# Performance work log

Measured on AMD Instinct MI355X. Metric: run time of the kernel, lower is better.

Reference implementation:

```python
import jax, jax.numpy as jnp
import numpy as np

D_MODEL, NHEAD, D_K = 512, 8, 64
MIN_RBF, MAX_RBF = 0.1, 0.9
MIN_SPREAD, MAX_SPREAD, BASE = 1.0, 6.0, 20.0
LN_EPS = 1e-5


def _layernorm(x, w, b):
    mu = jnp.mean(x, axis=-1, keepdims=True)
    var = jnp.var(x, axis=-1, keepdims=True)
    return (x - mu) * jax.lax.rsqrt(var + LN_EPS) * w + b


def setup_inputs() -> dict:
    key = jax.random.key(0)
    ks = jax.random.split(key, 10)
    B, N = 1, 2048
    inp = {
        "q": jax.random.normal(ks[0], (B, N, D_MODEL), jnp.float32),
        "k": jax.random.normal(ks[1], (B, N, D_MODEL), jnp.float32),
        "v": jax.random.normal(ks[2], (B, N, D_MODEL), jnp.float32),
        "coords": jax.random.normal(ks[3], (B, N, 3), jnp.float32) * 3.0,
        "key_padding_mask": jnp.zeros((B, N), bool),
        # learned params (torch.randn init for projections, LN defaults)
        "q_proj": jax.random.normal(ks[4], (NHEAD, D_MODEL, D_K), jnp.float32),
        "k_proj": jax.random.normal(ks[5], (NHEAD, D_MODEL, D_K), jnp.float32),
        "v_proj": jax.random.normal(ks[6], (NHEAD, D_MODEL, D_K), jnp.float32),
        "q_ln_w": jnp.ones((D_K,), jnp.float32), "q_ln_b": jnp.zeros((D_K,), jnp.float32),
        "k_ln_w": jnp.ones((D_K,), jnp.float32), "k_ln_b": jnp.zeros((D_K,), jnp.float32),
        "v_ln_w": jnp.ones((D_K,), jnp.float32), "v_ln_b": jnp.zeros((D_K,), jnp.float32),
        "out_w": jax.random.normal(ks[7], (D_MODEL, D_MODEL), jnp.float32) / np.sqrt(D_MODEL),
        "out_b": jnp.zeros((D_MODEL,), jnp.float32),
    }
    return inp


def reference(q, k, v, coords, key_padding_mask,
              q_proj, k_proj, v_proj,
              q_ln_w, q_ln_b, k_ln_w, k_ln_b, v_ln_w, v_ln_b,
              out_w, out_b):
    B, N, _ = q.shape
    # per-head projections: [B,H,N,dk]
    Q = _layernorm(jnp.einsum('bnd,hdk->bhnk', q, q_proj), q_ln_w, q_ln_b)
    K = _layernorm(jnp.einsum('bnd,hdk->bhnk', k, k_proj), k_ln_w, k_ln_b)
    V = _layernorm(jnp.einsum('bnd,hdk->bhnk', v, v_proj), v_ln_w, v_ln_b)

    # head-specific gaussian spreads (torch.logspace(0,1,H,base) semantics)
    spreads = MIN_SPREAD + (MAX_SPREAD - MIN_SPREAD) * (BASE ** jnp.linspace(0.0, 1.0, NHEAD) - 1.0) / (BASE - 1.0)

    # pairwise squared distances [B,N,N] -> per-head RBF [B,H,N,N]
    d2 = jnp.sum((coords[:, :, None, :] - coords[:, None, :, :]) ** 2, axis=-1)
    rbf = jnp.exp(-d2[:, None, :, :] / (2.0 * spreads[None, :, None, None] ** 2))
    rbf = jnp.clip(rbf, MIN_RBF, MAX_RBF)

    # RBF-modulated scaled dot-product attention
    scores = jnp.einsum('bhik,bhjk->bhij', Q, K) / np.sqrt(D_K) * rbf
    scores = jnp.where(key_padding_mask[:, None, None, :], -1e9, scores)
    P = jax.nn.softmax(scores, axis=-1)
    out = jnp.einsum('bhij,bhjk->bhik', P, V)  # [B,H,N,dk]

    # torch: out.permute(0,2,3,1).reshape(B,N,d_model)
    out = jnp.transpose(out, (0, 2, 3, 1)).reshape(B, N, D_MODEL)
    return out @ out_w.T + out_b
```

## Files before the change

### kernel.cpp

```cpp
#include <hip/hip_runtime.h>
#include <math.h>

#define N_TOK 2048
#define D_MODEL 512
#define NHEAD 8
#define DK 64
#define LOG2E 1.44269504f
#define QSCALE 0.18033688f

typedef __attribute__((ext_vector_type(8))) short short8;
typedef __attribute__((ext_vector_type(4))) short short4v;
typedef __attribute__((ext_vector_type(4))) float f32x4;

__device__ __forceinline__ short f2bf(float x) {
    unsigned u = __float_as_uint(x);
    u = (u + 0x7fffu + ((u >> 16) & 1u)) >> 16;
    return (short)u;
}

__device__ __forceinline__ unsigned cvt_pk_bf16(float lo, float hi) {
    unsigned r;
    asm("v_cvt_pk_bf16_f32 %0, %1, %2" : "=v"(r) : "v"(lo), "v"(hi));
    return r;
}

__device__ __forceinline__ float head_c(int h) {
    float tt = (float)h * (1.0f / 7.0f);
    float sp = 1.0f + 5.0f * (__builtin_exp2f(tt * 4.3219281f) - 1.0f) * (1.0f / 19.0f);
    return -LOG2E / (2.0f * sp * sp);
}

__global__ __launch_bounds__(256) void convert_x_kernel(
    const float* __restrict__ q, const float* __restrict__ k,
    const float* __restrict__ v, short* __restrict__ Xbf)
{
    int i = blockIdx.x * 256 + threadIdx.x;
    int t = i >> 17;
    int rem = i & 131071;
    const float4* src = (const float4*)(t == 0 ? q : (t == 1 ? k : v));
    float4 a = src[rem * 2], b = src[rem * 2 + 1];
    short8 o;
    o[0] = f2bf(a.x); o[1] = f2bf(a.y); o[2] = f2bf(a.z); o[3] = f2bf(a.w);
    o[4] = f2bf(b.x); o[5] = f2bf(b.y); o[6] = f2bf(b.z); o[7] = f2bf(b.w);
    *(short8*)(Xbf + (size_t)i * 8) = o;
}

__global__ __launch_bounds__(256) void prep_w_kernel(
    const float* __restrict__ qp, const float* __restrict__ kp,
    const float* __restrict__ vp, const float* __restrict__ ow,
    short* __restrict__ Wt, short* __restrict__ Wo)
{
    const int z = blockIdx.z, t = threadIdx.x;
    if (z == 3) {
        int m0 = blockIdx.x * 64, j0 = blockIdx.y * 64;
        for (int i = t; i < 4096; i += 256) {
            int r = i >> 6, c = i & 63;
            size_t idx = (size_t)(m0 + r) * 512 + j0 + c;
            Wo[idx] = f2bf(ow[idx]);
        }
        return;
    }
    const float* src = z == 0 ? qp : (z == 1 ? kp : vp);
    __shared__ float tile[64][65];
    const int h = blockIdx.x;
    const int d0 = blockIdx.y * 64;
    for (int i = t; i < 4096; i += 256) {
        int r = i >> 6, c = i & 63;
        tile[r][c] = src[((size_t)h * 512 + d0 + r) * 64 + c];
    }
    __syncthreads();
    short* W = Wt + (size_t)z * 512 * 512;
    for (int i = t; i < 4096; i += 256) {
        int cr = i >> 6, dc_ = i & 63;
        W[(size_t)(h * 64 + cr) * 512 + d0 + dc_] = f2bf(tile[dc_][cr]);
    }
}

__global__ __launch_bounds__(256) void prep_rbf_kernel(
    const float* __restrict__ coords, const unsigned char* __restrict__ mask,
    float4* __restrict__ ck4, float* __restrict__ mpen, unsigned* __restrict__ tflag)
{
    int j = blockIdx.x * 256 + threadIdx.x;
    float x = coords[j * 3 + 0], y = coords[j * 3 + 1], z = coords[j * 3 + 2];
    unsigned char mk = mask[j];
    mpen[j] = mk ? -1e9f : 0.f;
    unsigned long long b = __ballot(mk != 0);
    if ((threadIdx.x & 63) == 0) tflag[j >> 6] = (b != 0ull) ? 1u : 0u;
    float n2 = x * x + y * y + z * z;
    #pragma unroll
    for (int h = 0; h < NHEAD; ++h) {
        float c = head_c(h);
        float4 o; o.x = -2.f * c * x; o.y = -2.f * c * y; o.z = -2.f * c * z; o.w = c * n2;
        ck4[(size_t)h * N_TOK + j] = o;
    }
}

__global__ __launch_bounds__(256) void proj_ln_mfma_kernel(
    const short* __restrict__ Xbf, const short* __restrict__ Wt,
    const float* __restrict__ qlw, const float* __restrict__ qlb,
    const float* __restrict__ klw, const float* __restrict__ klb,
    const float* __restrict__ vlw, const float* __restrict__ vlb,
    short* __restrict__ Qbf, short* __restrict__ Kf, short* __restrict__ Vf)
{
    __shared__ short Xs[64 * 64];
    __shared__ short Ws[64 * 64];
    const int z = blockIdx.z, h = blockIdx.y;
    const int n0 = blockIdx.x * 64;
    const int tid = threadIdx.x, w = tid >> 6, l = tid & 63;
    const int l15 = l & 15, lg = l >> 4;

    const short* X = Xbf + (size_t)z * N_TOK * D_MODEL;
    const short* Wz = Wt + ((size_t)z * 512 + h * 64) * 512;

    const f32x4 zero4 = {0.f, 0.f, 0.f, 0.f};
    f32x4 acc[4];
    #pragma unroll
    for (int dc = 0; dc < 4; ++dc) acc[dc] = zero4;

    for (int kb = 0; kb < 8; ++kb) {
        const int d0 = kb * 64;
        __syncthreads();
        #pragma unroll
        for (int i = 0; i < 2; ++i) {
            int c = tid + i * 256;
            int r = c >> 3, g = c & 7;
            short8 xv = *(const short8*)(X + (size_t)(n0 + r) * 512 + d0 + g * 8);
            *(short8*)(Xs + r * 64 + ((g * 8) ^ ((r & 7) << 3))) = xv;
            short8 wv = *(const short8*)(Wz + (size_t)r * 512 + d0 + g * 8);
            *(short8*)(Ws + r * 64 + ((g * 8) ^ ((r & 7) << 3))) = wv;
        }
        __syncthreads();
        const int arow = w * 16 + l15;
        short8 a0 = *(const short8*)(Xs + arow * 64 + ((lg * 8) ^ ((arow & 7) << 3)));
        short8 a1 = *(const short8*)(Xs + arow * 64 + ((32 + lg * 8) ^ ((arow & 7) << 3)));
        #pragma unroll
        for (int dc = 0; dc < 4; ++dc) {
            const int brow = dc * 16 + l15;
            short8 b0 = *(const short8*)(Ws + brow * 64 + ((lg * 8) ^ ((brow & 7) << 3)));
            acc[dc] = __builtin_amdgcn_mfma_f32_16x16x32_bf16(a0, b0, acc[dc], 0, 0, 0);
            short8 b1 = *(const short8*)(Ws + brow * 64 + ((32 + lg * 8) ^ ((brow & 7) << 3)));
            acc[dc] = __builtin_amdgcn_mfma_f32_16x16x32_bf16(a1, b1, acc[dc], 0, 0, 0);
        }
    }

    const float* lw  = z == 0 ? qlw : (z == 1 ? klw : vlw);
    const float* lbp = z == 0 ? qlb : (z == 1 ? klb : vlb);
    float wv_[4], bv_[4];
    #pragma unroll
    for (int dc = 0; dc < 4; ++dc) {
        wv_[dc] = lw[dc * 16 + l15];
        bv_[dc] = lbp[dc * 16 + l15];
    }
    float mu[4], rs[4];
    #pragma unroll
    for (int reg = 0; reg < 4; ++reg) {
        float s = acc[0][reg] + acc[1][reg] + acc[2][reg] + acc[3][reg];
        #pragma unroll
        for (int off = 1; off < 16; off <<= 1) s += __shfl_xor(s, off);
        float m = s * (1.0f / 64.0f);
        float ss = 0.f;
        #pragma unroll
        for (int dc = 0; dc < 4; ++dc) { float d = acc[dc][reg] - m; ss += d * d; }
        #pragma unroll
        for (int off = 1; off < 16; off <<= 1) ss += __shfl_xor(ss, off);
        mu[reg] = m;
        rs[reg] = rsqrtf(ss * (1.0f / 64.0f) + 1e-5f);
    }

    const int tile = n0 >> 6;
    if (z == 0) {
        #pragma unroll
        for (int dc = 0; dc < 4; ++dc)
            #pragma unroll
            for (int reg = 0; reg < 4; ++reg) {
                int n = n0 + w * 16 + lg * 4 + reg;
                float val = ((acc[dc][reg] - mu[reg]) * rs[reg] * wv_[dc] + bv_[dc]) * QSCALE;
                Qbf[((size_t)h * N_TOK + n) * DK + dc * 16 + l15] = f2bf(val);
            }
    } else if (z == 1) {
        short* Kh = Kf + (size_t)h * N_TOK * DK;
        #pragma unroll
        for (int dc = 0; dc < 4; ++dc) {
            int hf  = dc >> 1;
            int lgc = ((dc & 1) << 1) | (l15 >> 3);
            int e   = l15 & 7;
            size_t base = (size_t)tile * 4096 + (w * 2 + hf) * 512 + 16 * 8 * lgc + e;
            #pragma unroll
            for (int reg = 0; reg < 4; ++reg) {
                float val = (acc[dc][reg] - mu[reg]) * rs[reg] * wv_[dc] + bv_[dc];
                Kh[base + (lg * 4 + reg) * 8] = f2bf(val);
            }
        }
    } else {
        short* Vh = Vf + (size_t)h * N_TOK * DK;
        int hfv = w >> 1;
        int lgv = ((w & 1) << 1) | (lg >> 1);
        int eb  = (lg & 1) * 4;
        #pragma unroll
        for (int dc = 0; dc < 4; ++dc) {
            short4v p;
            #pragma unroll
            for (int reg = 0; reg < 4; ++reg)
                p[reg] = f2bf((acc[dc][reg] - mu[reg]) * rs[reg] * wv_[dc] + bv_[dc]);
            size_t addr = (size_t)tile * 4096 + (dc * 2 + hfv) * 512 + (l15 + 16 * lgv) * 8 + eb;
            *(short4v*)(Vh + addr) = p;
        }
    }
}

__global__ __launch_bounds__(256) void attn_kernel(
    const short* __restrict__ Qbf, const short* __restrict__ Kf,
    const short* __restrict__ Vf, const float* __restrict__ coords,
    const float4* __restrict__ ck4, const float* __restrict__ mpen,
    const unsigned* __restrict__ tflag, short* __restrict__ att)
{
    __shared__ short Pls[4][1024];
    __shared__ float bufO[2][64][17];
    __shared__ float bufM[2][64];
    __shared__ float bufL[2][64];

    const int tid = threadIdx.x;
    const int w = tid >> 6, l = tid & 63;
    const int l15 = l & 15, lg = l >> 4;
    const int h = blockIdx.y;
    const int n0 = blockIdx.x * 16;

    char* Pb = (char*)&Pls[w][0];
    const int psw = (l15 & 7) << 4;

    const short* Qrow = Qbf + ((size_t)h * N_TOK + n0 + l15) * DK + lg * 8;
    const short8 qf0 = *(const short8*)(Qrow);
    const short8 qf1 = *(const short8*)(Qrow + 32);

    const float ch = head_c(h);
    const float qx = coords[(n0 + l15) * 3 + 0];
    const float qy = coords[(n0 + l15) * 3 + 1];
    const float qz = coords[(n0 + l15) * 3 + 2];
    const float cq2 = ch * (qx * qx + qy * qy + qz * qz);
    const float4* ckh = ck4 + (size_t)h * N_TOK;

    const f32x4 zero4 = {0.f, 0.f, 0.f, 0.f};
    float m_ = -INFINITY, l_ = 0.f;
    f32x4 oacc[4];
    #pragma unroll
    for (int i = 0; i < 4; ++i) oacc[i] = zero4;

    const short* Kfh = Kf + (size_t)h * N_TOK * DK;
    const short* Vfh = Vf + (size_t)h * N_TOK * DK;

    for (int t = 0; t < 8; ++t) {
        const int kt = w * 8 + t;
        const int kbase = kt * 64;
        const short* kp = Kfh + (size_t)kt * 4096 + l * 8;
        const short* vp = Vfh + (size_t)kt * 4096 + l * 8;

        f32x4 sacc[4];
        #pragma unroll
        for (int nc = 0; nc < 4; ++nc) {
            short8 k0 = *(const short8*)(kp + nc * 1024);
            short8 k1 = *(const short8*)(kp + nc * 1024 + 512);
            sacc[nc] = __builtin_amdgcn_mfma_f32_16x16x32_bf16(k0, qf0, zero4, 0, 0, 0);
            sacc[nc] = __builtin_amdgcn_mfma_f32_16x16x32_bf16(k1, qf1, sacc[nc], 0, 0, 0);
        }

        #pragma unroll
        for (int nc = 0; nc < 4; ++nc) {
            #pragma unroll
            for (int reg = 0; reg < 4; ++reg) {
                float4 c4 = ckh[kbase + nc * 16 + lg * 4 + reg];
                float arg = fmaf(c4.x, qx, fmaf(c4.y, qy, fmaf(c4.z, qz, c4.w))) + cq2;
                float rb = __builtin_exp2f(arg);
                rb = fminf(fmaxf(rb, 0.1f), 0.9f);
                sacc[nc][reg] *= rb;
            }
        }
        if (tflag[kt]) {
            #pragma unroll
            for (int nc = 0; nc < 4; ++nc)
                #pragma unroll
                for (int reg = 0; reg < 4; ++reg)
                    sacc[nc][reg] += mpen[kbase + nc * 16 + lg * 4 + reg];
        }

        float mx = -INFINITY;
        #pragma unroll
        for (int nc = 0; nc < 4; ++nc) {
            float a = fmaxf(sacc[nc][0], sacc[nc][1]);
            float b = fmaxf(sacc[nc][2], sacc[nc][3]);
            mx = fmaxf(mx, fmaxf(a, b));
        }
        mx = fmaxf(mx, __shfl_xor(mx, 16));
        mx = fmaxf(mx, __shfl_xor(mx, 32));

        if (!__all(mx <= m_ + 8.0f)) {
            float mn = fmaxf(m_, mx);
            float corr = __builtin_exp2f(m_ - mn);
            m_ = mn;
            l_ *= corr;
            #pragma unroll
            for (int dc = 0; dc < 4; ++dc) oacc[dc] *= corr;
        }

        float ps = 0.f;
        #pragma unroll
        for (int nc = 0; nc < 4; ++nc) {
            float p0 = __builtin_exp2f(sacc[nc][0] - m_);
            float p1 = __builtin_exp2f(sacc[nc][1] - m_);
            float p2 = __builtin_exp2f(sacc[nc][2] - m_);
            float p3 = __builtin_exp2f(sacc[nc][3] - m_);
            ps += (p0 + p1) + (p2 + p3);
            uint2 u;
            u.x = cvt_pk_bf16(p0, p1);
            u.y = cvt_pk_bf16(p2, p3);
            *(uint2*)(Pb + ((l15 * 128 + nc * 32 + lg * 8) ^ psw)) = u;
        }
        ps += __shfl_xor(ps, 16);
        ps += __shfl_xor(ps, 32);
        l_ += ps;

        short8 pf0 = *(const short8*)(Pb + ((l15 * 128 + lg * 16) ^ psw));
        short8 pf1 = *(const short8*)(Pb + ((l15 * 128 + 64 + lg * 16) ^ psw));
        #pragma unroll
        for (int dcc = 0; dcc < 4; ++dcc) {
            short8 v0 = *(const short8*)(vp + dcc * 1024);
            short8 v1 = *(const short8*)(vp + dcc * 1024 + 512);
            oacc[dcc] = __builtin_amdgcn_mfma_f32_16x16x32_bf16(v0, pf0, oacc[dcc], 0, 0, 0);
            oacc[dcc] = __builtin_amdgcn_mfma_f32_16x16x32_bf16(v1, pf1, oacc[dcc], 0, 0, 0);
        }
    }

    if (w >= 2) {
        int slot = w - 2;
        bufM[slot][l] = m_; bufL[slot][l] = l_;
        #pragma unroll
        for (int dc = 0; dc < 4; ++dc)
            #pragma unroll
            for (int reg = 0; reg < 4; ++reg)
                bufO[slot][l][dc * 4 + reg] = oacc[dc][reg];
    }
    __syncthreads();
    if (w < 2) {
        float mb = bufM[w][l], lb = bufL[w][l];
        float M = fmaxf(m_, mb);
        float fa = __builtin_exp2f(m_ - M), fb = __builtin_exp2f(mb - M);
        l_ = l_ * fa + lb * fb; m_ = M;
        #pragma unroll
        for (int dc = 0; dc < 4; ++dc)
            #pragma unroll
            for (int reg = 0; reg < 4; ++reg)
                oacc[dc][reg] = oacc[dc][reg] * fa + bufO[w][l][dc * 4 + reg] * fb;
    }
    __syncthreads();
    if (w == 1) {
        bufM[0][l] = m_; bufL[0][l] = l_;
        #pragma unroll
        for (int dc = 0; dc < 4; ++dc)
            #pragma unroll
            for (int reg = 0; reg < 4; ++reg)
                bufO[0][l][dc * 4 + reg] = oacc[dc][reg];
    }
    __syncthreads();
    if (w == 0) {
        float mb = bufM[0][l], lb = bufL[0][l];
        float M = fmaxf(m_, mb);
        float fa = __builtin_exp2f(m_ - M), fb = __builtin_exp2f(mb - M);
        l_ = l_ * fa + lb * fb;
        float rl = 1.0f / l_;
        #pragma unroll
        for (int dcc = 0; dcc < 4; ++dcc)
            #pragma unroll
            for (int reg = 0; reg < 4; ++reg) {
                float o = (oacc[dcc][reg] * fa + bufO[0][l][dcc * 4 + reg] * fb) * rl;
                att[(size_t)(n0 + l15) * D_MODEL + (dcc * 16 + lg * 4 + reg) * NHEAD + h] = f2bf(o);
            }
    }
}

__global__ __launch_bounds__(256) void out_proj_kernel(
    const short* __restrict__ ATT, const short* __restrict__ Wo,
    const float* __restrict__ bias, float* __restrict__ out)
{
    __shared__ short As[64 * 64];
    __shared__ short Bs[64 * 64];
    const int n0 = blockIdx.x * 64, m0 = blockIdx.y * 64;
    const int tid = threadIdx.x, w = tid >> 6, l = tid & 63;
    const int l15 = l & 15, lg = l >> 4;

    const f32x4 zero4 = {0.f, 0.f, 0.f, 0.f};
    f32x4 acc[4];
    #pragma unroll
    for (int dc = 0; dc < 4; ++dc) acc[dc] = zero4;

    for (int kb = 0; kb < 8; ++kb) {
        const int j0 = kb * 64;
        __syncthreads();
        #pragma unroll
        for (int i = 0; i < 2; ++i) {
            int c = tid + i * 256;
            int r = c >> 3, g = c & 7;
            short8 av = *(const short8*)(ATT + (size_t)(n0 + r) * 512 + j0 + g * 8);
            *(short8*)(As + r * 64 + ((g * 8) ^ ((r & 7) << 3))) = av;
            short8 bv = *(const short8*)(Wo + (size_t)(m0 + r) * 512 + j0 + g * 8);
            *(short8*)(Bs + r * 64 + ((g * 8) ^ ((r & 7) << 3))) = bv;
        }
        __syncthreads();
        const int arow = w * 16 + l15;
        short8 a0 = *(const short8*)(As + arow * 64 + ((lg * 8) ^ ((arow & 7) << 3)));
        short8 a1 = *(const short8*)(As + arow * 64 + ((32 + lg * 8) ^ ((arow & 7) << 3)));
        #pragma unroll
        for (int dc = 0; dc < 4; ++dc) {
            const int brow = dc * 16 + l15;
            short8 b0 = *(const short8*)(Bs + brow * 64 + ((lg * 8) ^ ((brow & 7) << 3)));
            acc[dc] = __builtin_amdgcn_mfma_f32_16x16x32_bf16(a0, b0, acc[dc], 0, 0, 0);
            short8 b1 = *(const short8*)(Bs + brow * 64 + ((32 + lg * 8) ^ ((brow & 7) << 3)));
            acc[dc] = __builtin_amdgcn_mfma_f32_16x16x32_bf16(a1, b1, acc[dc], 0, 0, 0);
        }
    }

    #pragma unroll
    for (int dc = 0; dc < 4; ++dc) {
        float bm = bias[m0 + dc * 16 + l15];
        #pragma unroll
        for (int reg = 0; reg < 4; ++reg) {
            int n = n0 + w * 16 + lg * 4 + reg;
            out[(size_t)n * D_MODEL + m0 + dc * 16 + l15] = acc[dc][reg] + bm;
        }
    }
}

extern "C" void kernel_launch(void* const* d_in, const int* in_sizes, int n_in,
                              void* d_out, int out_size, void* d_ws, size_t ws_size,
                              hipStream_t stream)
{
    const float* q      = (const float*)d_in[0];
    const float* k      = (const float*)d_in[1];
    const float* v      = (const float*)d_in[2];
    const float* coords = (const float*)d_in[3];
    const unsigned char* mask = (const unsigned char*)d_in[4];
    const float* q_proj = (const float*)d_in[5];
    const float* k_proj = (const float*)d_in[6];
    const float* v_proj = (const float*)d_in[7];
    const float* q_ln_w = (const float*)d_in[8];
    const float* q_ln_b = (const float*)d_in[9];
    const float* k_ln_w = (const float*)d_in[10];
    const float* k_ln_b = (const float*)d_in[11];
    const float* v_ln_w = (const float*)d_in[12];
    const float* v_ln_b = (const float*)d_in[13];
    const float* out_w  = (const float*)d_in[14];
    const float* out_b  = (const float*)d_in[15];
    float* out = (float*)d_out;

    short* Xbf = (short*)d_ws;
    short* Wt  = Xbf + 3145728;
    short* Wo  = Wt + 786432;
    short* Qbf = Wo + 262144;
    short* Kf  = Qbf + 1048576;
    short* Vf  = Kf + 1048576;
    short* ATT = Vf + 1048576;
    float*  fr   = (float*)(ATT + 1048576);
    float4* ck4  = (float4*)fr;
    float*  mpen = fr + 65536;
    unsigned* tflag = (unsigned*)(mpen + 2048);

    convert_x_kernel<<<dim3(1536), dim3(256), 0, stream>>>(q, k, v, Xbf);
    prep_w_kernel<<<dim3(8, 8, 4), dim3(256), 0, stream>>>(q_proj, k_proj, v_proj, out_w, Wt, Wo);
    prep_rbf_kernel<<<dim3(8), dim3(256), 0, stream>>>(coords, mask, ck4, mpen, tflag);
    proj_ln_mfma_kernel<<<dim3(32, 8, 3), dim3(256), 0, stream>>>(
        Xbf, Wt, q_ln_w, q_ln_b, k_ln_w, k_ln_b, v_ln_w, v_ln_b, Qbf, Kf, Vf);
    attn_kernel<<<dim3(128, 8), dim3(256), 0, stream>>>(Qbf, Kf, Vf, coords, ck4, mpen, tflag, ATT);
    out_proj_kernel<<<dim3(32, 8), dim3(256), 0, stream>>>(ATT, Wo, out_b, out);
}
```

Before: 74.86 us.

## Split attention over key halves and merge partials in a separate kernel

The attention kernel now runs with a grid z dimension of 2, so each block processes half of the key tiles. It writes unnormalized bf16 partial outputs plus the running max and sum, and a new merge kernel combines the two halves. The merged output is stored head-contiguous, and the out-projection weight is permuted to match, which replaces the strided scatter store. This doubles the number of attention blocks to raise occupancy and parallelism, at the cost of an extra launch, partial-result traffic through reused workspace, and extra bf16 rounding of the partial outputs.

```diff
diff --git a/kernel.cpp b/kernel.cpp
--- a/kernel.cpp
+++ b/kernel.cpp
@@ -16,6 +16,10 @@
     unsigned u = __float_as_uint(x);
     u = (u + 0x7fffu + ((u >> 16) & 1u)) >> 16;
     return (short)u;
+}
+
+__device__ __forceinline__ float bf2f(short s) {
+    return __uint_as_float(((unsigned)(unsigned short)s) << 16);
 }
 
 __device__ __forceinline__ unsigned cvt_pk_bf16(float lo, float hi) {
@@ -53,10 +57,11 @@
     const int z = blockIdx.z, t = threadIdx.x;
     if (z == 3) {
         int m0 = blockIdx.x * 64, j0 = blockIdx.y * 64;
+        int hh = j0 >> 6;
         for (int i = t; i < 4096; i += 256) {
-            int r = i >> 6, c = i & 63;
-            size_t idx = (size_t)(m0 + r) * 512 + j0 + c;
-            Wo[idx] = f2bf(ow[idx]);
+            int r = i >> 6, kk = i & 63;
+            Wo[(size_t)(m0 + r) * 512 + j0 + kk] =
+                f2bf(ow[(size_t)(m0 + r) * 512 + kk * 8 + hh]);
         }
         return;
     }
@@ -212,7 +217,8 @@
     const short* __restrict__ Qbf, const short* __restrict__ Kf,
     const short* __restrict__ Vf, const float* __restrict__ coords,
     const float4* __restrict__ ck4, const float* __restrict__ mpen,
-    const unsigned* __restrict__ tflag, short* __restrict__ att)
+    const unsigned* __restrict__ tflag,
+    short* __restrict__ PO, float* __restrict__ PM, float* __restrict__ PL)
 {
     __shared__ short Pls[4][1024];
     __shared__ float bufO[2][64][17];
@@ -223,6 +229,7 @@
     const int w = tid >> 6, l = tid & 63;
     const int l15 = l & 15, lg = l >> 4;
     const int h = blockIdx.y;
+    const int z = blockIdx.z;
     const int n0 = blockIdx.x * 16;
 
     char* Pb = (char*)&Pls[w][0];
@@ -248,8 +255,8 @@
     const short* Kfh = Kf + (size_t)h * N_TOK * DK;
     const short* Vfh = Vf + (size_t)h * N_TOK * DK;
 
-    for (int t = 0; t < 8; ++t) {
-        const int kt = w * 8 + t;
+    for (int t = 0; t < 4; ++t) {
+        const int kt = (z * 4 + w) * 4 + t;
         const int kbase = kt * 64;
         const short* kp = Kfh + (size_t)kt * 4096 + l * 8;
         const short* vp = Vfh + (size_t)kt * 4096 + l * 8;
@@ -364,16 +371,37 @@
         float mb = bufM[0][l], lb = bufL[0][l];
         float M = fmaxf(m_, mb);
         float fa = __builtin_exp2f(m_ - M), fb = __builtin_exp2f(mb - M);
-        l_ = l_ * fa + lb * fb;
-        float rl = 1.0f / l_;
-        #pragma unroll
-        for (int dcc = 0; dcc < 4; ++dcc)
-            #pragma unroll
-            for (int reg = 0; reg < 4; ++reg) {
-                float o = (oacc[dcc][reg] * fa + bufO[0][l][dcc * 4 + reg] * fb) * rl;
-                att[(size_t)(n0 + l15) * D_MODEL + (dcc * 16 + lg * 4 + reg) * NHEAD + h] = f2bf(o);
-            }
-    }
+        float lf = l_ * fa + lb * fb;
+        size_t p = ((size_t)z * NHEAD + h) * N_TOK + n0 + l15;
+        if (lg == 0) { PM[p] = M; PL[p] = lf; }
+        #pragma unroll
+        for (int dcc = 0; dcc < 4; ++dcc) {
+            short4v o4;
+            #pragma unroll
+            for (int reg = 0; reg < 4; ++reg)
+                o4[reg] = f2bf(oacc[dcc][reg] * fa + bufO[0][l][dcc * 4 + reg] * fb);
+            *(short4v*)(PO + p * 64 + dcc * 16 + lg * 4) = o4;
+        }
+    }
+}
+
+__global__ __launch_bounds__(256) void merge_kernel(
+    const short* __restrict__ PO, const float* __restrict__ PM,
+    const float* __restrict__ PL, short* __restrict__ ATT)
+{
+    const int t = threadIdx.x;
+    const int u = t >> 6, d = t & 63;
+    const int q = blockIdx.x * 4 + u;
+    const int h = blockIdx.y;
+    const size_t p0 = (size_t)h * N_TOK + q;
+    const size_t p1 = (size_t)(NHEAD + h) * N_TOK + q;
+    float m0 = PM[p0], m1 = PM[p1];
+    float l0 = PL[p0], l1 = PL[p1];
+    float M = fmaxf(m0, m1);
+    float f0 = __builtin_exp2f(m0 - M), f1 = __builtin_exp2f(m1 - M);
+    float rl = 1.0f / (l0 * f0 + l1 * f1);
+    float o0 = bf2f(PO[p0 * 64 + d]), o1 = bf2f(PO[p1 * 64 + d]);
+    ATT[(size_t)q * D_MODEL + h * 64 + d] = f2bf((o0 * f0 + o1 * f1) * rl);
 }
 
 __global__ __launch_bounds__(256) void out_proj_kernel(
@@ -462,11 +490,17 @@
     float*  mpen = fr + 65536;
     unsigned* tflag = (unsigned*)(mpen + 2048);
 
+    short* PO = Xbf;
+    float* PM = (float*)Wt;
+    float* PL = PM + 32768;
+
     convert_x_kernel<<<dim3(1536), dim3(256), 0, stream>>>(q, k, v, Xbf);
     prep_w_kernel<<<dim3(8, 8, 4), dim3(256), 0, stream>>>(q_proj, k_proj, v_proj, out_w, Wt, Wo);
     prep_rbf_kernel<<<dim3(8), dim3(256), 0, stream>>>(coords, mask, ck4, mpen, tflag);
     proj_ln_mfma_kernel<<<dim3(32, 8, 3), dim3(256), 0, stream>>>(
         Xbf, Wt, q_ln_w, q_ln_b, k_ln_w, k_ln_b, v_ln_w, v_ln_b, Qbf, Kf, Vf);
-    attn_kernel<<<dim3(128, 8), dim3(256), 0, stream>>>(Qbf, Kf, Vf, coords, ck4, mpen, tflag, ATT);
+    attn_kernel<<<dim3(128, 8, 2), dim3(256), 0, stream>>>(
+        Qbf, Kf, Vf, coords, ck4, mpen, tflag, PO, PM, PL);
+    merge_kernel<<<dim3(512, 8), dim3(256), 0, stream>>>(PO, PM, PL, ATT);
     out_proj_kernel<<<dim3(32, 8), dim3(256), 0, stream>>>(ATT, Wo, out_b, out);
 }
```

New measurement: 78.97 us. 1.05x slower.
